# Optimization experiments

Measured on AMD Instinct MI355X. Metric: run time of the kernel, lower is better.

Reference implementation:

```python
import jax, jax.numpy as jnp
from jax import lax
import numpy as np

B, C_IN, C_OUT, T, N, E = 4, 32, 32, 48, 2000, 16000


def _tconv(x, w, b):
    # Conv2d with kernel (3,1), padding (1,0): temporal conv over T, per-node.
    y = lax.conv_general_dilated(x, w, window_strides=(1, 1),
                                 padding=((1, 1), (0, 0)),
                                 dimension_numbers=('NCHW', 'OIHW', 'NCHW'))
    return y + b[None, :, None, None]


def setup_inputs() -> dict:
    key = jax.random.key(0)
    ks = jax.random.split(key, 8)
    x = jax.random.normal(ks[0], (B, C_IN, T, N), dtype=jnp.float32)
    edge_index = jax.random.randint(ks[1], (2, E), 0, N, dtype=jnp.int64)
    w1 = jax.random.normal(ks[2], (C_OUT, C_IN, 3, 1), dtype=jnp.float32) * 0.05
    b1 = jnp.zeros((C_OUT,), dtype=jnp.float32)
    gcn_w = jax.random.normal(ks[3], (C_OUT, C_OUT), dtype=jnp.float32) * 0.05
    gcn_b = jnp.zeros((C_OUT,), dtype=jnp.float32)
    w2 = jax.random.normal(ks[4], (C_OUT, C_OUT, 3, 1), dtype=jnp.float32) * 0.05
    b2 = jnp.zeros((C_OUT,), dtype=jnp.float32)
    return {"x": x, "edge_index": edge_index, "w1": w1, "b1": b1,
            "gcn_w": gcn_w, "gcn_b": gcn_b, "w2": w2, "b2": b2}


def reference(x, edge_index, w1, b1, gcn_w, gcn_b, w2, b2):
    # temporal conv 1 + relu
    h = jax.nn.relu(_tconv(x, w1, b1))          # [B, C, T, N]
    Bs, C, Ts, Ns = h.shape
    # replicate-graph GCN: same edge_index for all B*T graphs
    xf = h.transpose(0, 2, 3, 1).reshape(Bs * Ts, Ns, C)   # [BT, N, C]
    xw = xf @ gcn_w                                        # linear transform first
    src, dst = edge_index[0], edge_index[1]
    # GCN symmetric normalization with self-loops: deg = 1 + in-degree
    deg = jnp.zeros((Ns,), xw.dtype).at[dst].add(1.0) + 1.0
    dinv = lax.rsqrt(deg)
    wedge = dinv[src] * dinv[dst]                           # [E]

    def aggregate(g):  # g: [N, C] for one graph
        return jnp.zeros((Ns, C), g.dtype).at[dst].add(g[src] * wedge[:, None])

    agg = jax.vmap(aggregate)(xw)                           # [BT, N, C]
    out = agg + (1.0 / deg)[None, :, None] * xw + gcn_b     # self-loop term + bias
    out = out.reshape(Bs, Ts, Ns, C).transpose(0, 3, 1, 2)  # [B, C, T, N]
    # temporal conv 2
    return _tconv(out, w2, b2)
```

## Files before the change

### kernel.cpp

```cpp
#include <hip/hip_runtime.h>

#define BB 4
#define CIN 32
#define COUT 32
#define TT 48
#define NN 2000
#define EE 16000
#define BT (BB*TT)
#define PADCOL 24576


__global__ __launch_bounds__(256) void k_zero(int* __restrict__ col,
                                              float* __restrict__ wedge,
                                              int* __restrict__ gcnt) {
    int i = blockIdx.x * 256 + threadIdx.x;
    if (i < PADCOL) { col[i] = 0; wedge[i] = 0.f; }
    if (i < 2048)   gcnt[i] = 0;
}


__global__ __launch_bounds__(256) void k_count(const int* __restrict__ ei,
                                               int* __restrict__ gcnt) {
    int e = blockIdx.x * 256 + threadIdx.x;
    if (e < EE) atomicAdd(&gcnt[ei[EE + e]], 1);
}


__global__ __launch_bounds__(1024) void k_build(
        const int* __restrict__ gcnt,
        const float* __restrict__ w1, const float* __restrict__ gw,
        const float* __restrict__ gb, const float* __restrict__ w2,
        const float* __restrict__ cb2,
        int* __restrict__ rowptr, float* __restrict__ dinv2,
        float* __restrict__ dinvg, int* __restrict__ fillptr,
        float* __restrict__ w1t, float* __restrict__ w2c,
        float* __restrict__ biasE) {
    __shared__ int   cnt[2048];
    __shared__ int   buf[2048];
    __shared__ float sw2t[3072];
    __shared__ float sgw[1024];
    __shared__ float sbk[96];
    int t = threadIdx.x;

    for (int i = t; i < 3072; i += 1024) {
        int c = i & 31, r = i >> 5;
        int co = r & 31, k = r >> 5;
        sw2t[i] = w2[c * 96 + co * 3 + k];
        w1t[i]  = w1[c * 96 + co * 3 + k];
    }
    sgw[t] = gw[t];
    cnt[t] = gcnt[t]; cnt[t + 1024] = gcnt[t + 1024];
    __syncthreads();

    for (int i = t; i < 2048; i += 1024)
        buf[i] = (i < NN) ? ((cnt[i] + 3) & ~3) : 0;
    __syncthreads();
    for (int s = 1; s < 2048; s <<= 1) {
        int i0 = t, i1 = t + 1024;
        int a0 = buf[i0] + ((i0 >= s) ? buf[i0 - s] : 0);
        int a1 = buf[i1] + ((i1 >= s) ? buf[i1 - s] : 0);
        __syncthreads();
        buf[i0] = a0; buf[i1] = a1;
        __syncthreads();
    }

    for (int i = t; i < 2048; i += 1024) {
        if (i < NN) {
            rowptr[i + 1] = buf[i];
            float deg = (float)(cnt[i] + 1);
            dinvg[i] = rsqrtf(deg);
            dinv2[i] = 1.0f / deg;
            fillptr[i] = buf[i] - ((cnt[i] + 3) & ~3);
        }
    }
    if (t == 0) rowptr[0] = 0;

    for (int i = t; i < 3072; i += 1024) {
        int c = i & 31, r = i >> 5;
        int cm = r & 31, k = r >> 5;
        float acc = 0.f;
#pragma unroll
        for (int co = 0; co < 32; co++)
            acc += sgw[cm * 32 + co] * sw2t[(k * 32 + co) * 32 + c];
        w2c[i] = acc;
    }
    for (int i = t; i < 96; i += 1024) {
        int k = i >> 5, c = i & 31;
        float acc = 0.f;
#pragma unroll
        for (int co = 0; co < 32; co++)
            acc += gb[co] * sw2t[(k * 32 + co) * 32 + c];
        sbk[i] = acc;
    }
    __syncthreads();
    for (int i = t; i < 96; i += 1024) {
        int cls = i >> 5, c = i & 31;
        float v = cb2[c] + sbk[32 + c];
        if (cls != 0) v += sbk[c];
        if (cls != 2) v += sbk[64 + c];
        biasE[i] = v;
    }
}


__global__ void k_fill(const int* __restrict__ ei, int* __restrict__ fillptr,
                       const float* __restrict__ dinvg,
                       int* __restrict__ col, float* __restrict__ wedge) {
    int e = blockIdx.x * blockDim.x + threadIdx.x;
    if (e < EE) {
        int s = ei[e], d = ei[EE + e];
        int pos = atomicAdd(fillptr + d, 1);
        col[pos]   = s;
        wedge[pos] = dinvg[s] * dinvg[d];
    }
}


__global__ __launch_bounds__(256) void k_conv1(const float* __restrict__ x,
                                               const float* __restrict__ w1t,
                                               const float* __restrict__ b1,
                                               float* __restrict__ hbuf) {
    __shared__ float ls[256 * 36];
    int bid = blockIdx.x;
    int xcd = bid & 7;
    int i   = bid >> 3;
    int nch = i & 7;
    int r   = i >> 3;
    int tloc = r % 6, b = r / 6;
    int t = xcd * 6 + tloc;
    int tid = threadIdx.x;
    int n0 = nch * 256;
    int n  = n0 + tid;
    int nvalid = (NN - n0 < 256) ? (NN - n0) : 256;
    int n_eff = (n < NN) ? n : (NN - 1);
    int g = b * TT + t;
    int gb = g >> 3, gsub = g & 7;

    float ha[COUT];
#pragma unroll
    for (int c = 0; c < COUT; c++) ha[c] = b1[c];

    const float* xbase = x + ((size_t)b * CIN * TT) * NN + n_eff;
    bool hasL = (t > 0), hasR = (t < TT - 1);
    const float* pL = xbase + (size_t)(hasL ? t - 1 : 0) * NN;
    const float* pM = xbase + (size_t)t * NN;
    const float* pR = xbase + (size_t)(hasR ? t + 1 : 0) * NN;

    float xa[CIN], xm[CIN];
#pragma unroll
    for (int ci = 0; ci < CIN; ci++) xa[ci] = pL[(size_t)ci * TT * NN];
#pragma unroll
    for (int ci = 0; ci < CIN; ci++) xm[ci] = pM[(size_t)ci * TT * NN];
    __builtin_amdgcn_sched_barrier(0);

    if (hasL) {
        const float* wp = w1t;
#pragma unroll
        for (int ci = 0; ci < CIN; ci++) {
#pragma unroll
            for (int c = 0; c < COUT; c++) ha[c] += xa[ci] * wp[ci * COUT + c];
        }
    }
    __builtin_amdgcn_sched_barrier(0);

#pragma unroll
    for (int ci = 0; ci < CIN; ci++) xa[ci] = pR[(size_t)ci * TT * NN];
    __builtin_amdgcn_sched_barrier(0);

    {
        const float* wp = w1t + 1024;
#pragma unroll
        for (int ci = 0; ci < CIN; ci++) {
#pragma unroll
            for (int c = 0; c < COUT; c++) ha[c] += xm[ci] * wp[ci * COUT + c];
        }
    }
    __builtin_amdgcn_sched_barrier(0);

    if (hasR) {
        const float* wp = w1t + 2048;
#pragma unroll
        for (int ci = 0; ci < CIN; ci++) {
#pragma unroll
            for (int c = 0; c < COUT; c++) ha[c] += xa[ci] * wp[ci * COUT + c];
        }
    }

#pragma unroll
    for (int q = 0; q < 8; q++) {
        *(float4*)&ls[tid * 36 + q * 4] =
            make_float4(fmaxf(ha[4*q], 0.f), fmaxf(ha[4*q+1], 0.f),
                        fmaxf(ha[4*q+2], 0.f), fmaxf(ha[4*q+3], 0.f));
    }
    __syncthreads();

    size_t hb0 = (((size_t)gb * NN + n0) * 8 + gsub) * 32;
#pragma unroll
    for (int q = 0; q < 8; q++) {
        int f = q * 256 + tid;
        int c = f >> 3;
        int s = f & 7;
        if (c < nvalid)
            *(float4*)(hbuf + hb0 + (size_t)c * 256 + s * 4) =
                *(float4*)&ls[c * 36 + s * 4];
    }
}


__global__ __launch_bounds__(256) void k_agg(const float* __restrict__ hbuf,
                                             const int* __restrict__ rowptr,
                                             const int* __restrict__ col,
                                             const float* __restrict__ wedge,
                                             const float* __restrict__ dinv2,
                                             float* __restrict__ gbuf) {
    int bid = blockIdx.x;
    int xcd = bid & 7;
    int q   = bid >> 3;
    int gbr = q / 500;
    int nch = q % 500;
    int gb  = gbr * 8 + xcd;
    int wid  = threadIdx.x >> 6;
    int lane = threadIdx.x & 63;
    int gsub = lane >> 3;
    int cq   = lane & 7;
    int n    = nch * 4 + wid;

    const float* xg = hbuf + (size_t)gb * NN * 256;
    size_t loff = (size_t)gsub * 32 + cq * 4;

    float4 self = *(const float4*)(xg + (size_t)n * 256 + loff);
    float dv = dinv2[n];
    float4 acc = make_float4(dv * self.x, dv * self.y, dv * self.z, dv * self.w);

    int j  = rowptr[n];
    int je = rowptr[n + 1];
    for (; j < je; j += 4) {
        int4   cc = *(const int4*)(col + j);
        float4 ww = *(const float4*)(wedge + j);
        float4 v0 = *(const float4*)(xg + (size_t)cc.x * 256 + loff);
        float4 v1 = *(const float4*)(xg + (size_t)cc.y * 256 + loff);
        float4 v2 = *(const float4*)(xg + (size_t)cc.z * 256 + loff);
        float4 v3 = *(const float4*)(xg + (size_t)cc.w * 256 + loff);
        acc.x += ww.x*v0.x + ww.y*v1.x + ww.z*v2.x + ww.w*v3.x;
        acc.y += ww.x*v0.y + ww.y*v1.y + ww.z*v2.y + ww.w*v3.y;
        acc.z += ww.x*v0.z + ww.y*v1.z + ww.z*v2.z + ww.w*v3.z;
        acc.w += ww.x*v0.w + ww.y*v1.w + ww.z*v2.w + ww.w*v3.w;
    }

    int g = gb * 8 + gsub;
    *(float4*)(gbuf + ((size_t)g * NN + n) * 32 + cq * 4) = acc;
}


#define LD32(GV, GP) { \
    _Pragma("unroll") \
    for (int q_ = 0; q_ < 8; q_++) { \
        float4 v_ = (GP)[q_]; \
        GV[4*q_] = v_.x; GV[4*q_+1] = v_.y; GV[4*q_+2] = v_.z; GV[4*q_+3] = v_.w; } }

#define FMA32(ACC, GV, WP) { \
    _Pragma("unroll") \
    for (int cm_ = 0; cm_ < 32; cm_++) { \
        float g_ = GV[cm_]; \
        _Pragma("unroll") \
        for (int c_ = 0; c_ < 32; c_++) ACC[c_] += g_ * (WP)[cm_ * 32 + c_]; } }

__global__ __launch_bounds__(256) void k_conv2(const float* __restrict__ gbuf,
                                               const float* __restrict__ w2c,
                                               const float* __restrict__ biasE,
                                               float* __restrict__ out) {
    int bid  = blockIdx.x;
    int xcd  = bid & 7;
    int slot = bid >> 3;
    int grp  = xcd * 24 + (slot >> 3);
    int nch  = slot & 7;
    int b = grp / TT;
    int t = grp % TT;
    int n = nch * 256 + threadIdx.x;
    if (n >= NN) return;

    bool hasL = (t > 0), hasR = (t < TT - 1);
    const float4* pL = (const float4*)(gbuf + (((size_t)(b * TT + (hasL ? t - 1 : 0))) * NN + n) * CIN);
    const float4* pM = (const float4*)(gbuf + (((size_t)(b * TT + t)) * NN + n) * CIN);
    const float4* pR = (const float4*)(gbuf + (((size_t)(b * TT + (hasR ? t + 1 : 0))) * NN + n) * CIN);

    float o[COUT];
#pragma unroll
    for (int c = 0; c < COUT; c++) o[c] = 0.f;

    float ga[CIN], gm[CIN];
    LD32(ga, pL);
    LD32(gm, pM);
    __builtin_amdgcn_sched_barrier(0);

    if (hasL) { FMA32(o, ga, w2c); }
    __builtin_amdgcn_sched_barrier(0);

    LD32(ga, pR);
    __builtin_amdgcn_sched_barrier(0);

    FMA32(o, gm, w2c + 1024);
    __builtin_amdgcn_sched_barrier(0);

    if (hasR) { FMA32(o, ga, w2c + 2048); }

    int cls = (t == 0) ? 0 : ((t == TT - 1) ? 2 : 1);
    const float* bp = biasE + cls * 32;
#pragma unroll
    for (int c = 0; c < COUT; c++)
        out[(((size_t)b * COUT + c) * TT + t) * NN + n] = o[c] + bp[c];
}


extern "C" void kernel_launch(void* const* d_in, const int* in_sizes, int n_in,
                              void* d_out, int out_size, void* d_ws, size_t ws_size,
                              hipStream_t stream) {
    const float* x     = (const float*)d_in[0];
    const int*   ei    = (const int*)d_in[1];
    const float* w1    = (const float*)d_in[2];
    const float* b1    = (const float*)d_in[3];
    const float* gcn_w = (const float*)d_in[4];
    const float* gcn_b = (const float*)d_in[5];
    const float* w2    = (const float*)d_in[6];
    const float* b2    = (const float*)d_in[7];
    float* out = (float*)d_out;

    const size_t XWB = (size_t)BT * NN * COUT * sizeof(float);
    char* w = (char*)d_ws;
    float* hbuf    = (float*)w;  w += XWB;
    float* gbuf    = (float*)w;  w += XWB;
    int*   rowptr  = (int*)w;    w += 8192;
    float* dinv2   = (float*)w;  w += 8192;
    float* dinvg   = (float*)w;  w += 8192;
    int*   fillptr = (int*)w;    w += 8192;
    int*   gcnt    = (int*)w;    w += 8192;
    int*   col     = (int*)w;    w += PADCOL * sizeof(int);
    float* wedge   = (float*)w;  w += PADCOL * sizeof(float);
    float* w1t     = (float*)w;  w += 3072 * sizeof(float);
    float* w2c     = (float*)w;  w += 3072 * sizeof(float);
    float* biasE   = (float*)w;  w += 96 * sizeof(float);

    k_zero <<<dim3((PADCOL + 255) / 256), dim3(256), 0, stream>>>(col, wedge, gcnt);
    k_count<<<dim3((EE + 255) / 256), dim3(256), 0, stream>>>(ei, gcnt);
    k_build<<<dim3(1), dim3(1024), 0, stream>>>(gcnt, w1, gcn_w, gcn_b, w2, b2,
                                                rowptr, dinv2, dinvg, fillptr,
                                                w1t, w2c, biasE);
    k_fill <<<dim3((EE + 255) / 256), dim3(256), 0, stream>>>(ei, fillptr, dinvg, col, wedge);
    k_conv1<<<dim3(1536), dim3(256), 0, stream>>>(x, w1t, b1, hbuf);
    k_agg  <<<dim3(12000), dim3(256), 0, stream>>>(hbuf, rowptr, col, wedge, dinv2, gbuf);
    k_conv2<<<dim3(1536), dim3(256), 0, stream>>>(gbuf, w2c, biasE, out);
}
```

Baseline: 235.1 us.

## Compute two timesteps per thread in conv1 to reuse input loads

Each conv1 thread now produces two adjacent output timesteps, so it loads four input time slices instead of six for two outputs, and the grid is halved. The LDS staging and block barrier for the output transpose are removed; each thread writes its 32-channel rows directly as float4 stores. The cost is higher register pressure from two accumulator arrays, fewer blocks, and per-thread strided stores that may coalesce less well than the old staged writes.

```diff
diff --git a/kernel.cpp b/kernel.cpp
--- a/kernel.cpp
+++ b/kernel.cpp
@@ -120,89 +120,109 @@
                                                const float* __restrict__ w1t,
                                                const float* __restrict__ b1,
                                                float* __restrict__ hbuf) {
-    __shared__ float ls[256 * 36];
     int bid = blockIdx.x;
     int xcd = bid & 7;
     int i   = bid >> 3;
     int nch = i & 7;
     int r   = i >> 3;
-    int tloc = r % 6, b = r / 6;
-    int t = xcd * 6 + tloc;
-    int tid = threadIdx.x;
-    int n0 = nch * 256;
-    int n  = n0 + tid;
-    int nvalid = (NN - n0 < 256) ? (NN - n0) : 256;
-    int n_eff = (n < NN) ? n : (NN - 1);
-    int g = b * TT + t;
-    int gb = g >> 3, gsub = g & 7;
-
-    float ha[COUT];
-#pragma unroll
-    for (int c = 0; c < COUT; c++) ha[c] = b1[c];
-
-    const float* xbase = x + ((size_t)b * CIN * TT) * NN + n_eff;
-    bool hasL = (t > 0), hasR = (t < TT - 1);
-    const float* pL = xbase + (size_t)(hasL ? t - 1 : 0) * NN;
-    const float* pM = xbase + (size_t)t * NN;
-    const float* pR = xbase + (size_t)(hasR ? t + 1 : 0) * NN;
-
-    float xa[CIN], xm[CIN];
-#pragma unroll
-    for (int ci = 0; ci < CIN; ci++) xa[ci] = pL[(size_t)ci * TT * NN];
-#pragma unroll
-    for (int ci = 0; ci < CIN; ci++) xm[ci] = pM[(size_t)ci * TT * NN];
-    __builtin_amdgcn_sched_barrier(0);
+    int tploc = r % 3, b = r / 3;
+    int tp = xcd * 3 + tploc;
+    int t0 = tp * 2;
+    int n = nch * 256 + threadIdx.x;
+    if (n >= NN) return;
+
+    float ha0[COUT], ha1[COUT];
+#pragma unroll
+    for (int c = 0; c < COUT; c++) { ha0[c] = b1[c]; ha1[c] = b1[c]; }
+
+    const float* xbase = x + ((size_t)b * CIN * TT) * NN + n;
+    bool hasL = (t0 > 0);
+    bool hasR = (t0 + 2 < TT);
+
+    float xt[CIN];
 
     if (hasL) {
+        const float* p = xbase + (size_t)(t0 - 1) * NN;
+#pragma unroll
+        for (int ci = 0; ci < CIN; ci++) xt[ci] = p[(size_t)ci * TT * NN];
+        __builtin_amdgcn_sched_barrier(0);
         const float* wp = w1t;
 #pragma unroll
         for (int ci = 0; ci < CIN; ci++) {
-#pragma unroll
-            for (int c = 0; c < COUT; c++) ha[c] += xa[ci] * wp[ci * COUT + c];
-        }
-    }
-    __builtin_amdgcn_sched_barrier(0);
-
-#pragma unroll
-    for (int ci = 0; ci < CIN; ci++) xa[ci] = pR[(size_t)ci * TT * NN];
-    __builtin_amdgcn_sched_barrier(0);
+            float v = xt[ci];
+#pragma unroll
+            for (int c = 0; c < COUT; c++) ha0[c] += v * wp[ci * COUT + c];
+        }
+    }
 
     {
-        const float* wp = w1t + 1024;
+        const float* p = xbase + (size_t)t0 * NN;
+#pragma unroll
+        for (int ci = 0; ci < CIN; ci++) xt[ci] = p[(size_t)ci * TT * NN];
+        __builtin_amdgcn_sched_barrier(0);
 #pragma unroll
         for (int ci = 0; ci < CIN; ci++) {
-#pragma unroll
-            for (int c = 0; c < COUT; c++) ha[c] += xm[ci] * wp[ci * COUT + c];
-        }
-    }
-    __builtin_amdgcn_sched_barrier(0);
+            float v = xt[ci];
+            const float* w1p = w1t + 1024 + ci * COUT;
+            const float* w0p = w1t + ci * COUT;
+#pragma unroll
+            for (int c = 0; c < COUT; c++) {
+                ha0[c] += v * w1p[c];
+                ha1[c] += v * w0p[c];
+            }
+        }
+    }
+
+    {
+        const float* p = xbase + (size_t)(t0 + 1) * NN;
+#pragma unroll
+        for (int ci = 0; ci < CIN; ci++) xt[ci] = p[(size_t)ci * TT * NN];
+        __builtin_amdgcn_sched_barrier(0);
+#pragma unroll
+        for (int ci = 0; ci < CIN; ci++) {
+            float v = xt[ci];
+            const float* w2p = w1t + 2048 + ci * COUT;
+            const float* w1p = w1t + 1024 + ci * COUT;
+#pragma unroll
+            for (int c = 0; c < COUT; c++) {
+                ha0[c] += v * w2p[c];
+                ha1[c] += v * w1p[c];
+            }
+        }
+    }
+
+    {
+        int g = b * TT + t0;
+        int gb = g >> 3, gsub = g & 7;
+        float4* pa = (float4*)(hbuf + (((size_t)gb * NN + n) * 8 + gsub) * 32);
+#pragma unroll
+        for (int q = 0; q < 8; q++)
+            pa[q] = make_float4(fmaxf(ha0[4*q], 0.f), fmaxf(ha0[4*q+1], 0.f),
+                                fmaxf(ha0[4*q+2], 0.f), fmaxf(ha0[4*q+3], 0.f));
+    }
 
     if (hasR) {
+        const float* p = xbase + (size_t)(t0 + 2) * NN;
+#pragma unroll
+        for (int ci = 0; ci < CIN; ci++) xt[ci] = p[(size_t)ci * TT * NN];
+        __builtin_amdgcn_sched_barrier(0);
         const float* wp = w1t + 2048;
 #pragma unroll
         for (int ci = 0; ci < CIN; ci++) {
-#pragma unroll
-            for (int c = 0; c < COUT; c++) ha[c] += xa[ci] * wp[ci * COUT + c];
-        }
-    }
-
-#pragma unroll
-    for (int q = 0; q < 8; q++) {
-        *(float4*)&ls[tid * 36 + q * 4] =
-            make_float4(fmaxf(ha[4*q], 0.f), fmaxf(ha[4*q+1], 0.f),
-                        fmaxf(ha[4*q+2], 0.f), fmaxf(ha[4*q+3], 0.f));
-    }
-    __syncthreads();
-
-    size_t hb0 = (((size_t)gb * NN + n0) * 8 + gsub) * 32;
-#pragma unroll
-    for (int q = 0; q < 8; q++) {
-        int f = q * 256 + tid;
-        int c = f >> 3;
-        int s = f & 7;
-        if (c < nvalid)
-            *(float4*)(hbuf + hb0 + (size_t)c * 256 + s * 4) =
-                *(float4*)&ls[c * 36 + s * 4];
+            float v = xt[ci];
+#pragma unroll
+            for (int c = 0; c < COUT; c++) ha1[c] += v * wp[ci * COUT + c];
+        }
+    }
+
+    {
+        int g = b * TT + t0 + 1;
+        int gb = g >> 3, gsub = g & 7;
+        float4* pa = (float4*)(hbuf + (((size_t)gb * NN + n) * 8 + gsub) * 32);
+#pragma unroll
+        for (int q = 0; q < 8; q++)
+            pa[q] = make_float4(fmaxf(ha1[4*q], 0.f), fmaxf(ha1[4*q+1], 0.f),
+                                fmaxf(ha1[4*q+2], 0.f), fmaxf(ha1[4*q+3], 0.f));
     }
 }
 
@@ -346,7 +366,7 @@
                                                 rowptr, dinv2, dinvg, fillptr,
                                                 w1t, w2c, biasE);
     k_fill <<<dim3((EE + 255) / 256), dim3(256), 0, stream>>>(ei, fillptr, dinvg, col, wedge);
-    k_conv1<<<dim3(1536), dim3(256), 0, stream>>>(x, w1t, b1, hbuf);
+    k_conv1<<<dim3(768), dim3(256), 0, stream>>>(x, w1t, b1, hbuf);
     k_agg  <<<dim3(12000), dim3(256), 0, stream>>>(hbuf, rowptr, col, wedge, dinv2, gbuf);
     k_conv2<<<dim3(1536), dim3(256), 0, stream>>>(gbuf, w2c, biasE, out);
 }
```

Result: slower. 246.8 us (+5.0%).
